# Kernel tuning notes

Measured on AMD Instinct MI355X. Metric: run time of the kernel, lower is better.

Reference implementation:

```python
import jax, jax.numpy as jnp
import numpy as np

B, YS, XS, H = 16, 256, 256, 128  # batch, image height (y_size), width (x_size), MLP hidden


def setup_inputs() -> dict:
    key = jax.random.key(0)
    ks = jax.random.split(key, 6)
    images = jax.random.normal(ks[0], (B, YS, XS), dtype=jnp.float32)

    def glorot(k, shape):
        fan_in = shape[0]
        return (jax.random.normal(k, shape, dtype=jnp.float32) / np.float32(np.sqrt(fan_in)))

    W1 = glorot(ks[1], (3, H));  b1 = jnp.zeros((H,), jnp.float32)
    W2 = glorot(ks[2], (H, H));  b2 = jnp.zeros((H,), jnp.float32)
    W3 = glorot(ks[3], (H, H));  b3 = jnp.zeros((H,), jnp.float32)
    W4 = glorot(ks[4], (H, 1));  b4 = jnp.zeros((1,), jnp.float32)
    return {
        "images": images,
        "W1": W1, "b1": b1, "W2": W2, "b2": b2,
        "W3": W3, "b3": b3, "W4": W4, "b4": b4,
        "diffusion_weight": jnp.float32(0.1),
        "n": 0,
    }


def reference(images, W1, b1, W2, b2, W3, b3, W4, b4, diffusion_weight, n):
    # NOTE: in the original torch module, diffusion_loss (and all autograd
    # derivatives) are computed but never added to total_loss; only
    # boundary_loss accumulates. We reproduce exactly that math.
    Bn, y_size, x_size = images.shape
    x = jnp.linspace(-x_size / 2, x_size / 2, x_size, dtype=images.dtype)
    y = jnp.linspace(-y_size / 2, y_size / 2, y_size, dtype=images.dtype)
    Xg, Yg = jnp.meshgrid(x, y, indexing="ij")  # (x_size, y_size), x-major
    xf = Xg.ravel()  # (N,) with N = x_size*y_size
    yf = Yg.ravel()

    # t_recon is all-zeros in the original, so T_recon_i = i + n*B (constant field).
    ts = jnp.arange(Bn, dtype=images.dtype) + jnp.asarray(n * Bn, images.dtype)  # (B,)

    def field(tval):
        tf = jnp.zeros_like(xf) + tval
        inp = jnp.stack([xf, yf, tf], axis=-1)          # (N, 3)
        h = jnp.tanh(inp @ W1 + b1)
        h = jnp.tanh(h @ W2 + b2)
        h = jnp.tanh(h @ W3 + b3)
        return (h @ W4 + b4)[:, 0]                       # (N,)

    surface_recon = jax.vmap(field)(ts)                  # (B, N)
    # matches torch: surface_recon.view(y_size, x_size) on the ij-flattened field
    recon = surface_recon.reshape(Bn, y_size, x_size)
    boundary = jnp.mean((images - recon) ** 2, axis=(1, 2))  # per-sample
    return jnp.sum(boundary) / Bn
```

## Files before the change

### kernel.cpp

```cpp
#include <hip/hip_runtime.h>
#include <hip/hip_bf16.h>


#define BATCH 16
#define LDA 136
#define STEP (256.0f / 255.0f)
#define KS 2.8853900817779268f

typedef __bf16 v8bf __attribute__((ext_vector_type(8)));
typedef float  v4f  __attribute__((ext_vector_type(4)));

__device__ __forceinline__ unsigned short f2bf(float f) {
    unsigned int u = __float_as_uint(f);
    unsigned int r = (u + 0x7fffu + ((u >> 16) & 1u)) >> 16;
    return (unsigned short)r;
}

#if __has_builtin(__builtin_amdgcn_perm)
__device__ __forceinline__ unsigned int pack2bf(float a, float b) {
    return __builtin_amdgcn_perm(__float_as_uint(b), __float_as_uint(a), 0x07060302u);
}
#else
__device__ __forceinline__ unsigned int pack2bf(float a, float b) {
    return (__float_as_uint(a) >> 16) | (__float_as_uint(b) & 0xffff0000u);
}
#endif

__device__ __forceinline__ float tanh_pre(float zk) {
    float e = __builtin_amdgcn_exp2f(zk);
    float r = __builtin_amdgcn_rcpf(e + 1.f);
    return fmaf(-2.f, r, 1.f);
}

__global__ __launch_bounds__(256) void prep_kernel(
    const float* __restrict__ W2, const float* __restrict__ W3,
    unsigned short* __restrict__ w2t, unsigned short* __restrict__ w3t,
    float* __restrict__ partials, unsigned int* __restrict__ counter)
{
    __shared__ float t[32][33];

    const int bid = blockIdx.x;
    const int tid = threadIdx.x;

    {
        int o = bid * 256 + tid;
        if (o < 1024) partials[o] = 0.f;
        if (o == 0) *counter = 0u;
    }

    const float* src          = (bid < 16) ? W2 : W3;
    unsigned short* dst       = (bid < 16) ? w2t : w3t;
    const int tl = bid & 15;
    const int tr = tl >> 2;
    const int tc = tl & 3;
    const int tx = tid & 31;
    const int ty = tid >> 5;

    #pragma unroll
    for (int i = 0; i < 4; ++i) {
        int a = i * 8 + ty;
        t[a][tx] = src[(tr * 32 + a) * 128 + tc * 32 + tx];
    }
    __syncthreads();

    #pragma unroll
    for (int i = 0; i < 4; ++i) {
        int nn = tc * 32 + i * 8 + ty;
        int kk = tr * 32 + tx;
        dst[nn * 128 + kk] = f2bf(t[tx][i * 8 + ty] * KS);
    }
}

__global__ __launch_bounds__(512, 8) void main_kernel(
    const float* __restrict__ images,
    const float* __restrict__ W1, const float* __restrict__ b1,
    const float* __restrict__ b2, const float* __restrict__ b3,
    const float* __restrict__ W4, const float* __restrict__ b4,
    const int*   __restrict__ np,
    const unsigned short* __restrict__ w2t,
    const unsigned short* __restrict__ w3t,
    float* __restrict__ partials, unsigned int* __restrict__ counter,
    float* __restrict__ out)
{
    __shared__ unsigned short A[128 * LDA];
    __shared__ float P[8][128];
    __shared__ float red[8];
    __shared__ unsigned int isLastS;

    const int tid  = threadIdx.x;
    const int lane = tid & 63;
    const int w    = tid >> 6;
    const int l15  = lane & 15;
    const int quad = lane >> 4;

    const int bid = blockIdx.x;
    const int b   = bid >> 9;
    const int rem = bid & 511;
    const int r   = rem >> 1;
    const int c0  = (rem & 1) << 7;

    const float tv = (float)(b + np[0] * BATCH);
    const float xv = -128.f + (float)r * STEP;

    {
        const int lo = tid & 31, hi = tid >> 5;
        const int j0 = lo * 4, p0 = hi * 8;
        float4 wx = *(const float4*)(W1 + j0);
        float4 wy = *(const float4*)(W1 + 128 + j0);
        float4 wt = *(const float4*)(W1 + 256 + j0);
        float4 bb = *(const float4*)(b1 + j0);
        const float yv0 = fmaf((float)(c0 + p0), STEP, -128.f);
        float z0 = fmaf(yv0, KS * wy.x, KS * fmaf(xv, wx.x, fmaf(tv, wt.x, bb.x)));
        float z1 = fmaf(yv0, KS * wy.y, KS * fmaf(xv, wx.y, fmaf(tv, wt.y, bb.y)));
        float z2 = fmaf(yv0, KS * wy.z, KS * fmaf(xv, wx.z, fmaf(tv, wt.z, bb.z)));
        float z3 = fmaf(yv0, KS * wy.w, KS * fmaf(xv, wx.w, fmaf(tv, wt.w, bb.w)));
        float e0 = __builtin_amdgcn_exp2f(z0);
        float e1 = __builtin_amdgcn_exp2f(z1);
        float e2 = __builtin_amdgcn_exp2f(z2);
        float e3 = __builtin_amdgcn_exp2f(z3);
        const float E0 = __builtin_amdgcn_exp2f(KS * STEP * wy.x);
        const float E1 = __builtin_amdgcn_exp2f(KS * STEP * wy.y);
        const float E2 = __builtin_amdgcn_exp2f(KS * STEP * wy.z);
        const float E3 = __builtin_amdgcn_exp2f(KS * STEP * wy.w);
        #pragma unroll
        for (int pi = 0; pi < 8; ++pi) {
            float h0 = fmaf(-2.f, __builtin_amdgcn_rcpf(e0 + 1.f), 1.f);
            float h1 = fmaf(-2.f, __builtin_amdgcn_rcpf(e1 + 1.f), 1.f);
            float h2 = fmaf(-2.f, __builtin_amdgcn_rcpf(e2 + 1.f), 1.f);
            float h3 = fmaf(-2.f, __builtin_amdgcn_rcpf(e3 + 1.f), 1.f);
            uint2 u = make_uint2(pack2bf(h0, h1), pack2bf(h2, h3));
            *(uint2*)&A[(p0 + pi) * LDA + j0] = u;
            e0 *= E0; e1 *= E1; e2 *= E2; e3 *= E3;
        }
    }
    __syncthreads();

    const int colw = w * 16 + l15;
    const int ch4  = w * 16 + quad * 4;

    v8bf wf[4];
    #pragma unroll
    for (int ks = 0; ks < 4; ++ks)
        wf[ks] = *(const v8bf*)(w2t + colw * 128 + ks * 32 + quad * 8);

    v4f acc[8];
    {
        float4 b2q = *(const float4*)(b2 + ch4);
        v4f ini = (v4f){b2q.x * KS, b2q.y * KS, b2q.z * KS, b2q.w * KS};
        #pragma unroll
        for (int mt = 0; mt < 8; ++mt) acc[mt] = ini;
    }
    #pragma unroll
    for (int ks = 0; ks < 4; ++ks) {
        #pragma unroll
        for (int mt = 0; mt < 8; ++mt) {
            v8bf af = *(const v8bf*)&A[(mt * 16 + l15) * LDA + ks * 32 + quad * 8];
            acc[mt] = __builtin_amdgcn_mfma_f32_16x16x32_bf16(wf[ks], af, acc[mt], 0, 0, 0);
        }
    }

    v8bf w3f[4];
    #pragma unroll
    for (int ks = 0; ks < 4; ++ks)
        w3f[ks] = *(const v8bf*)(w3t + colw * 128 + ks * 32 + quad * 8);
    __syncthreads();

    #pragma unroll
    for (int mt = 0; mt < 8; ++mt) {
        uint2 u = make_uint2(pack2bf(tanh_pre(acc[mt][0]), tanh_pre(acc[mt][1])),
                             pack2bf(tanh_pre(acc[mt][2]), tanh_pre(acc[mt][3])));
        *(uint2*)&A[(mt * 16 + l15) * LDA + ch4] = u;
    }
    __syncthreads();

    {
        float4 b3q = *(const float4*)(b3 + ch4);
        v4f ini = (v4f){b3q.x * KS, b3q.y * KS, b3q.z * KS, b3q.w * KS};
        #pragma unroll
        for (int mt = 0; mt < 8; ++mt) acc[mt] = ini;
    }
    #pragma unroll
    for (int ks = 0; ks < 4; ++ks) {
        #pragma unroll
        for (int mt = 0; mt < 8; ++mt) {
            v8bf af = *(const v8bf*)&A[(mt * 16 + l15) * LDA + ks * 32 + quad * 8];
            acc[mt] = __builtin_amdgcn_mfma_f32_16x16x32_bf16(w3f[ks], af, acc[mt], 0, 0, 0);
        }
    }

    {
        float4 w4q = *(const float4*)(W4 + ch4);
        #pragma unroll
        for (int mt = 0; mt < 8; ++mt) {
            float s;
            s  = tanh_pre(acc[mt][0]) * w4q.x;
            s  = fmaf(tanh_pre(acc[mt][1]), w4q.y, s);
            s  = fmaf(tanh_pre(acc[mt][2]), w4q.z, s);
            s  = fmaf(tanh_pre(acc[mt][3]), w4q.w, s);
            s += __shfl_xor(s, 16, 64);
            s += __shfl_xor(s, 32, 64);
            if (quad == 0) P[w][mt * 16 + l15] = s;
        }
    }
    __syncthreads();

    {
        float e2 = 0.f;
        if (tid < 128) {
            float s = b4[0];
            #pragma unroll
            for (int ww = 0; ww < 8; ++ww) s += P[ww][tid];
            float img = images[(b << 16) + (r << 8) + c0 + tid];
            float err = img - s;
            e2 = err * err;
        }
        #pragma unroll
        for (int off = 1; off < 64; off <<= 1)
            e2 += __shfl_xor(e2, off, 64);
        if (lane == 0 && tid < 128)
            atomicAdd(&partials[bid & 1023], e2);
    }

    __syncthreads();
    if (tid == 0)
        isLastS = (atomicAdd(counter, 1u) == (unsigned)(gridDim.x - 1)) ? 1u : 0u;
    __syncthreads();
    if (isLastS) {
        float s = __hip_atomic_load(&partials[tid],       __ATOMIC_RELAXED, __HIP_MEMORY_SCOPE_AGENT)
                + __hip_atomic_load(&partials[tid + 512], __ATOMIC_RELAXED, __HIP_MEMORY_SCOPE_AGENT);
        #pragma unroll
        for (int off = 1; off < 64; off <<= 1)
            s += __shfl_xor(s, off, 64);
        if (lane == 0) red[w] = s;
        __syncthreads();
        if (tid == 0) {
            float tot = 0.f;
            #pragma unroll
            for (int i = 0; i < 8; ++i) tot += red[i];
            out[0] = tot * (1.f / 1048576.f);
        }
    }
}

extern "C" void kernel_launch(void* const* d_in, const int* in_sizes, int n_in,
                              void* d_out, int out_size, void* d_ws, size_t ws_size,
                              hipStream_t stream)
{
    const float* images = (const float*)d_in[0];
    const float* W1 = (const float*)d_in[1];
    const float* b1 = (const float*)d_in[2];
    const float* W2 = (const float*)d_in[3];
    const float* b2 = (const float*)d_in[4];
    const float* W3 = (const float*)d_in[5];
    const float* b3 = (const float*)d_in[6];
    const float* W4 = (const float*)d_in[7];
    const float* b4 = (const float*)d_in[8];
    const int*   np = (const int*)d_in[10];

    unsigned short* w2t = (unsigned short*)d_ws;
    unsigned short* w3t = w2t + 128 * 128;
    float* partials = (float*)((char*)d_ws + 65536);
    unsigned int* counter = (unsigned int*)((char*)d_ws + 65536 + 4096);

    prep_kernel<<<32, 256, 0, stream>>>(W2, W3, w2t, w3t, partials, counter);
    main_kernel<<<BATCH * 256 * 2, 512, 0, stream>>>(
        images, W1, b1, b2, b3, W4, b4, np, w2t, w3t, partials, counter, (float*)d_out);
}
```

Baseline: 194.3 us.

## Halve block tile to 64 points with 256 threads and two channel groups per wave

```diff
diff --git a/kernel.cpp b/kernel.cpp
--- a/kernel.cpp
+++ b/kernel.cpp
@@ -71,7 +71,7 @@
     }
 }
 
-__global__ __launch_bounds__(512, 8) void main_kernel(
+__global__ __launch_bounds__(256, 8) void main_kernel(
     const float* __restrict__ images,
     const float* __restrict__ W1, const float* __restrict__ b1,
     const float* __restrict__ b2, const float* __restrict__ b3,
@@ -82,9 +82,9 @@
     float* __restrict__ partials, unsigned int* __restrict__ counter,
     float* __restrict__ out)
 {
-    __shared__ unsigned short A[128 * LDA];
-    __shared__ float P[8][128];
-    __shared__ float red[8];
+    __shared__ unsigned short A[64 * LDA];
+    __shared__ float P[4][64];
+    __shared__ float red[4];
     __shared__ unsigned int isLastS;
 
     const int tid  = threadIdx.x;
@@ -94,10 +94,10 @@
     const int quad = lane >> 4;
 
     const int bid = blockIdx.x;
-    const int b   = bid >> 9;
-    const int rem = bid & 511;
-    const int r   = rem >> 1;
-    const int c0  = (rem & 1) << 7;
+    const int b   = bid >> 10;
+    const int rem = bid & 1023;
+    const int r   = rem >> 2;
+    const int c0  = (rem & 3) << 6;
 
     const float tv = (float)(b + np[0] * BATCH);
     const float xv = -128.f + (float)r * STEP;
@@ -135,68 +135,78 @@
     }
     __syncthreads();
 
-    const int colw = w * 16 + l15;
-    const int ch4  = w * 16 + quad * 4;
-
-    v8bf wf[4];
-    #pragma unroll
-    for (int ks = 0; ks < 4; ++ks)
-        wf[ks] = *(const v8bf*)(w2t + colw * 128 + ks * 32 + quad * 8);
-
-    v4f acc[8];
+    v4f acc[2][4];
+    #pragma unroll
+    for (int g = 0; g < 2; ++g) {
+        const int colw = w * 32 + g * 16 + l15;
+        const int ch4  = w * 32 + g * 16 + quad * 4;
+        v8bf wf[4];
+        #pragma unroll
+        for (int ks = 0; ks < 4; ++ks)
+            wf[ks] = *(const v8bf*)(w2t + colw * 128 + ks * 32 + quad * 8);
+        float4 bq = *(const float4*)(b2 + ch4);
+        v4f ini = (v4f){bq.x * KS, bq.y * KS, bq.z * KS, bq.w * KS};
+        #pragma unroll
+        for (int mt = 0; mt < 4; ++mt) acc[g][mt] = ini;
+        #pragma unroll
+        for (int ks = 0; ks < 4; ++ks) {
+            #pragma unroll
+            for (int mt = 0; mt < 4; ++mt) {
+                v8bf af = *(const v8bf*)&A[(mt * 16 + l15) * LDA + ks * 32 + quad * 8];
+                acc[g][mt] = __builtin_amdgcn_mfma_f32_16x16x32_bf16(wf[ks], af, acc[g][mt], 0, 0, 0);
+            }
+        }
+    }
+    __syncthreads();
+
+    #pragma unroll
+    for (int g = 0; g < 2; ++g) {
+        const int ch4 = w * 32 + g * 16 + quad * 4;
+        #pragma unroll
+        for (int mt = 0; mt < 4; ++mt) {
+            uint2 u = make_uint2(pack2bf(tanh_pre(acc[g][mt][0]), tanh_pre(acc[g][mt][1])),
+                                 pack2bf(tanh_pre(acc[g][mt][2]), tanh_pre(acc[g][mt][3])));
+            *(uint2*)&A[(mt * 16 + l15) * LDA + ch4] = u;
+        }
+    }
+    __syncthreads();
+
+    #pragma unroll
+    for (int g = 0; g < 2; ++g) {
+        const int colw = w * 32 + g * 16 + l15;
+        const int ch4  = w * 32 + g * 16 + quad * 4;
+        v8bf wf[4];
+        #pragma unroll
+        for (int ks = 0; ks < 4; ++ks)
+            wf[ks] = *(const v8bf*)(w3t + colw * 128 + ks * 32 + quad * 8);
+        float4 bq = *(const float4*)(b3 + ch4);
+        v4f ini = (v4f){bq.x * KS, bq.y * KS, bq.z * KS, bq.w * KS};
+        #pragma unroll
+        for (int mt = 0; mt < 4; ++mt) acc[g][mt] = ini;
+        #pragma unroll
+        for (int ks = 0; ks < 4; ++ks) {
+            #pragma unroll
+            for (int mt = 0; mt < 4; ++mt) {
+                v8bf af = *(const v8bf*)&A[(mt * 16 + l15) * LDA + ks * 32 + quad * 8];
+                acc[g][mt] = __builtin_amdgcn_mfma_f32_16x16x32_bf16(wf[ks], af, acc[g][mt], 0, 0, 0);
+            }
+        }
+    }
+
     {
-        float4 b2q = *(const float4*)(b2 + ch4);
-        v4f ini = (v4f){b2q.x * KS, b2q.y * KS, b2q.z * KS, b2q.w * KS};
-        #pragma unroll
-        for (int mt = 0; mt < 8; ++mt) acc[mt] = ini;
-    }
-    #pragma unroll
-    for (int ks = 0; ks < 4; ++ks) {
-        #pragma unroll
-        for (int mt = 0; mt < 8; ++mt) {
-            v8bf af = *(const v8bf*)&A[(mt * 16 + l15) * LDA + ks * 32 + quad * 8];
-            acc[mt] = __builtin_amdgcn_mfma_f32_16x16x32_bf16(wf[ks], af, acc[mt], 0, 0, 0);
-        }
-    }
-
-    v8bf w3f[4];
-    #pragma unroll
-    for (int ks = 0; ks < 4; ++ks)
-        w3f[ks] = *(const v8bf*)(w3t + colw * 128 + ks * 32 + quad * 8);
-    __syncthreads();
-
-    #pragma unroll
-    for (int mt = 0; mt < 8; ++mt) {
-        uint2 u = make_uint2(pack2bf(tanh_pre(acc[mt][0]), tanh_pre(acc[mt][1])),
-                             pack2bf(tanh_pre(acc[mt][2]), tanh_pre(acc[mt][3])));
-        *(uint2*)&A[(mt * 16 + l15) * LDA + ch4] = u;
-    }
-    __syncthreads();
-
-    {
-        float4 b3q = *(const float4*)(b3 + ch4);
-        v4f ini = (v4f){b3q.x * KS, b3q.y * KS, b3q.z * KS, b3q.w * KS};
-        #pragma unroll
-        for (int mt = 0; mt < 8; ++mt) acc[mt] = ini;
-    }
-    #pragma unroll
-    for (int ks = 0; ks < 4; ++ks) {
-        #pragma unroll
-        for (int mt = 0; mt < 8; ++mt) {
-            v8bf af = *(const v8bf*)&A[(mt * 16 + l15) * LDA + ks * 32 + quad * 8];
-            acc[mt] = __builtin_amdgcn_mfma_f32_16x16x32_bf16(w3f[ks], af, acc[mt], 0, 0, 0);
-        }
-    }
-
-    {
-        float4 w4q = *(const float4*)(W4 + ch4);
-        #pragma unroll
-        for (int mt = 0; mt < 8; ++mt) {
+        float4 w4a = *(const float4*)(W4 + w * 32 + quad * 4);
+        float4 w4b = *(const float4*)(W4 + w * 32 + 16 + quad * 4);
+        #pragma unroll
+        for (int mt = 0; mt < 4; ++mt) {
             float s;
-            s  = tanh_pre(acc[mt][0]) * w4q.x;
-            s  = fmaf(tanh_pre(acc[mt][1]), w4q.y, s);
-            s  = fmaf(tanh_pre(acc[mt][2]), w4q.z, s);
-            s  = fmaf(tanh_pre(acc[mt][3]), w4q.w, s);
+            s = tanh_pre(acc[0][mt][0]) * w4a.x;
+            s = fmaf(tanh_pre(acc[0][mt][1]), w4a.y, s);
+            s = fmaf(tanh_pre(acc[0][mt][2]), w4a.z, s);
+            s = fmaf(tanh_pre(acc[0][mt][3]), w4a.w, s);
+            s = fmaf(tanh_pre(acc[1][mt][0]), w4b.x, s);
+            s = fmaf(tanh_pre(acc[1][mt][1]), w4b.y, s);
+            s = fmaf(tanh_pre(acc[1][mt][2]), w4b.z, s);
+            s = fmaf(tanh_pre(acc[1][mt][3]), w4b.w, s);
             s += __shfl_xor(s, 16, 64);
             s += __shfl_xor(s, 32, 64);
             if (quad == 0) P[w][mt * 16 + l15] = s;
@@ -204,20 +214,15 @@
     }
     __syncthreads();
 
-    {
-        float e2 = 0.f;
-        if (tid < 128) {
-            float s = b4[0];
-            #pragma unroll
-            for (int ww = 0; ww < 8; ++ww) s += P[ww][tid];
-            float img = images[(b << 16) + (r << 8) + c0 + tid];
-            float err = img - s;
-            e2 = err * err;
-        }
+    if (tid < 64) {
+        float s = b4[0] + P[0][tid] + P[1][tid] + P[2][tid] + P[3][tid];
+        float img = images[(b << 16) + (r << 8) + c0 + tid];
+        float err = img - s;
+        float e2 = err * err;
         #pragma unroll
         for (int off = 1; off < 64; off <<= 1)
             e2 += __shfl_xor(e2, off, 64);
-        if (lane == 0 && tid < 128)
+        if (lane == 0)
             atomicAdd(&partials[bid & 1023], e2);
     }
 
@@ -227,16 +232,16 @@
     __syncthreads();
     if (isLastS) {
         float s = __hip_atomic_load(&partials[tid],       __ATOMIC_RELAXED, __HIP_MEMORY_SCOPE_AGENT)
-                + __hip_atomic_load(&partials[tid + 512], __ATOMIC_RELAXED, __HIP_MEMORY_SCOPE_AGENT);
+                + __hip_atomic_load(&partials[tid + 256], __ATOMIC_RELAXED, __HIP_MEMORY_SCOPE_AGENT)
+                + __hip_atomic_load(&partials[tid + 512], __ATOMIC_RELAXED, __HIP_MEMORY_SCOPE_AGENT)
+                + __hip_atomic_load(&partials[tid + 768], __ATOMIC_RELAXED, __HIP_MEMORY_SCOPE_AGENT);
         #pragma unroll
         for (int off = 1; off < 64; off <<= 1)
             s += __shfl_xor(s, off, 64);
         if (lane == 0) red[w] = s;
         __syncthreads();
         if (tid == 0) {
-            float tot = 0.f;
-            #pragma unroll
-            for (int i = 0; i < 8; ++i) tot += red[i];
+            float tot = (red[0] + red[1]) + (red[2] + red[3]);
             out[0] = tot * (1.f / 1048576.f);
         }
     }
@@ -263,6 +268,6 @@
     unsigned int* counter = (unsigned int*)((char*)d_ws + 65536 + 4096);
 
     prep_kernel<<<32, 256, 0, stream>>>(W2, W3, w2t, w3t, partials, counter);
-    main_kernel<<<BATCH * 256 * 2, 512, 0, stream>>>(
+    main_kernel<<<BATCH * 256 * 4, 256, 0, stream>>>(
         images, W1, b1, b2, b3, W4, b4, np, w2t, w3t, partials, counter, (float*)d_out);
 }
```

New measurement: 307.5 us. +58.3%, slower.
